# Kernel optimization log

Measured on AMD Instinct MI355X. Metric: run time of the kernel, lower is better.

## Reference

```python
import jax, jax.numpy as jnp
import numpy as np

# Module hyper-params (match init_kwargs)
IN_C, OUT_C = 64, 64
KH, KW = 3, 3            # kernel_size_2d
UNIT = 16                # unit_size (width of virtual 2D feature map)
K = KH * KW              # equivalent 1D kernel size = 9
PAD = (K - 1) // 2       # = 4


def _tap_positions(T):
    # Fixed integer deform-conv offsets: tap j in group g = j // KW gets
    # x-offset (UNIT - KW) * (g - center_group).
    center = (KH - 1) // 2
    off = np.array([(UNIT - KW) * (j // KW - center) for j in range(K)], dtype=np.int32)
    # deform-conv sample position for output t, tap j (stride=1, dilation=1):
    #   pos = t - PAD + j + off[j]
    pos = np.arange(T, dtype=np.int32)[None, :] - PAD + np.arange(K, dtype=np.int32)[:, None] + off[:, None]  # [K, T]
    valid = (pos >= 0) & (pos < T)
    return np.clip(pos, 0, T - 1), valid


def setup_inputs() -> dict:
    key = jax.random.key(0)
    k1, k2, k3 = jax.random.split(key, 3)
    B, T = 8, 65536
    x = jax.random.normal(k1, (B, IN_C, T), dtype=jnp.float32)
    # weight init: uniform(-stdv, stdv), stdv = 1/sqrt(in_c * 1 * K)
    stdv = 1.0 / float(np.sqrt(IN_C * K))
    weight = jax.random.uniform(k2, (OUT_C, IN_C, K), jnp.float32, -stdv, stdv)
    # bias init: uniform(-bound, bound), bound = 1/sqrt(fan_in) = stdv
    bias = jax.random.uniform(k3, (OUT_C,), jnp.float32, -stdv, stdv)
    return {"x": x, "weight": weight, "bias": bias}


def reference(x, weight, bias):
    B, C, T = x.shape
    pos, valid = _tap_positions(T)
    pos = jnp.asarray(pos)
    valid = jnp.asarray(valid)
    # integer gather (offsets are integer so bilinear sampling is exact), zero outside
    xg = jnp.where(valid[None, None], x[:, :, pos], 0.0)  # [B, C, K, T]
    out = jnp.einsum('ock,bckt->bot', weight, xg)          # [B, OUT_C, T]
    return out + bias[None, :, None]
```

## Files before the change

### kernel.cpp

```cpp
#include <hip/hip_runtime.h>


typedef short bf16x8 __attribute__((ext_vector_type(8)));
typedef short bf16x4 __attribute__((ext_vector_type(4)));
typedef float f32x4  __attribute__((ext_vector_type(4)));

#define T_LEN   65536
#define NT      128
#define ROWS    168
#define PITCH   68
#define LOFF    20
#define NCHUNK  18
#define OPITCH  132
#define XS_BYTES (ROWS * PITCH * 2)
#define OS_BYTES (32 * OPITCH * 4)
#define SMEM_BYTES XS_BYTES

__device__ __forceinline__ short f2bf(float f) {
    union { float f; unsigned u; } v; v.f = f;
    unsigned u = v.u;
    u += 0x7fffu + ((u >> 16) & 1u);
    return (short)(u >> 16);
}

__global__ void prep_w_kernel(const float* __restrict__ w, short* __restrict__ W2) {
    int idx = blockIdx.x * 256 + threadIdx.x;
    if (idx >= 4 * NCHUNK * 64) return;
    int lane = idx & 63;
    int g    = idx >> 6;
    int ch   = g >> 2;
    int mt   = g & 3;
    int o    = mt * 16 + (lane & 15);
    bf16x8 v;
#pragma unroll
    for (int i = 0; i < 8; ++i) {
        int kk = ch * 32 + (lane >> 4) * 8 + i;
        int j = kk >> 6, c = kk & 63;
        v[i] = f2bf(w[o * 576 + c * 9 + j]);
    }
    *(bf16x8*)(W2 + (size_t)idx * 8) = v;
}

__global__ __launch_bounds__(256, 4)
void ta_main_kernel(const float* __restrict__ x, const short* __restrict__ W2,
                    const float* __restrict__ bias, float* __restrict__ out) {
    __shared__ __align__(16) char smem[SMEM_BYTES];
    short* xs = (short*)smem;
    float* os = (float*)smem;

    const int tid  = threadIdx.x;
    const int wv   = tid >> 6;
    const int lane = tid & 63;
    const int l15  = lane & 15;
    const int quad = lane >> 4;
    const int b    = blockIdx.y;
    const int bxd  = blockIdx.x;
    const int bx   = (bxd & 7) * 64 + (bxd >> 3);
    const int t0   = bx * NT;

    const int c = tid >> 2;
    const int q = tid & 3;
    const float* xrow = x + (((size_t)(b * 64 + c)) << 16);
    const int tbase = t0 - LOFF;
    const bool interior = (t0 >= LOFF) && (t0 + (ROWS - LOFF) <= T_LEN);

    if (interior) {
        f32x4 v[11];
#pragma unroll
        for (int i = 0; i < 11; ++i) {
            const int f = q + 4 * i;
            if (f < 42) v[i] = *(const f32x4*)(xrow + tbase + 4 * f);
        }
#pragma unroll
        for (int i = 0; i < 11; ++i) {
            const int f = q + 4 * i;
            if (f < 42) {
                const int tt = 4 * f;
                xs[(tt + 0) * PITCH + c] = f2bf(v[i][0]);
                xs[(tt + 1) * PITCH + c] = f2bf(v[i][1]);
                xs[(tt + 2) * PITCH + c] = f2bf(v[i][2]);
                xs[(tt + 3) * PITCH + c] = f2bf(v[i][3]);
            }
        }
    } else {
#pragma unroll
        for (int i = 0; i < 11; ++i) {
            const int f = q + 4 * i;
            if (f < 42) {
                const int tt = 4 * f;
                const int tg = tbase + tt;
                f32x4 v;
                v[0] = ((unsigned)(tg + 0) < (unsigned)T_LEN) ? xrow[tg + 0] : 0.f;
                v[1] = ((unsigned)(tg + 1) < (unsigned)T_LEN) ? xrow[tg + 1] : 0.f;
                v[2] = ((unsigned)(tg + 2) < (unsigned)T_LEN) ? xrow[tg + 2] : 0.f;
                v[3] = ((unsigned)(tg + 3) < (unsigned)T_LEN) ? xrow[tg + 3] : 0.f;
                xs[(tt + 0) * PITCH + c] = f2bf(v[0]);
                xs[(tt + 1) * PITCH + c] = f2bf(v[1]);
                xs[(tt + 2) * PITCH + c] = f2bf(v[2]);
                xs[(tt + 3) * PITCH + c] = f2bf(v[3]);
            }
        }
    }
    __syncthreads();

    int bbase[2];
#pragma unroll
    for (int nt = 0; nt < 2; ++nt) {
        const int tl = wv * 32 + nt * 16 + l15;
        bbase[nt] = (tl + 3) * PITCH + quad * 8;
    }
    const short* w2p = W2 + (size_t)lane * 8;

    f32x4 acc[4][2] = {};

    const int dtab[9] = {-17, -16, -15, -1, 0, 1, 15, 16, 17};

    bf16x8 a_cur[4], b_cur[2], a_nxt[4], b_nxt[2];

    {
        const int roff0 = (dtab[0] + 17) * PITCH + 0;
#pragma unroll
        for (int mt = 0; mt < 4; ++mt)
            a_cur[mt] = *(const bf16x8*)(w2p + (size_t)(0 * 4 + mt) * 512);
#pragma unroll
        for (int nt = 0; nt < 2; ++nt) {
            union { bf16x8 v8; bf16x4 v4[2]; } u;
            u.v4[0] = *(const bf16x4*)(xs + bbase[nt] + roff0);
            u.v4[1] = *(const bf16x4*)(xs + bbase[nt] + roff0 + 4);
            b_cur[nt] = u.v8;
        }
    }

#pragma unroll
    for (int ch = 0; ch < NCHUNK; ++ch) {
        if (ch < NCHUNK - 1) {
            const int chn = ch + 1;
            const int jn = chn >> 1, hn = chn & 1;
            const int roffn = (dtab[jn] + 17) * PITCH + hn * 32;
#pragma unroll
            for (int mt = 0; mt < 4; ++mt)
                a_nxt[mt] = *(const bf16x8*)(w2p + (size_t)(chn * 4 + mt) * 512);
#pragma unroll
            for (int nt = 0; nt < 2; ++nt) {
                union { bf16x8 v8; bf16x4 v4[2]; } u;
                u.v4[0] = *(const bf16x4*)(xs + bbase[nt] + roffn);
                u.v4[1] = *(const bf16x4*)(xs + bbase[nt] + roffn + 4);
                b_nxt[nt] = u.v8;
            }
        }
#pragma unroll
        for (int mt = 0; mt < 4; ++mt)
#pragma unroll
            for (int nt = 0; nt < 2; ++nt)
                acc[mt][nt] = __builtin_amdgcn_mfma_f32_16x16x32_bf16(a_cur[mt], b_cur[nt], acc[mt][nt], 0, 0, 0);
        if (ch < NCHUNK - 1) {
#pragma unroll
            for (int mt = 0; mt < 4; ++mt) a_cur[mt] = a_nxt[mt];
#pragma unroll
            for (int nt = 0; nt < 2; ++nt) b_cur[nt] = b_nxt[nt];
        }
    }

    const size_t outb = ((size_t)(b * 64)) << 16;
#pragma unroll
    for (int p = 0; p < 2; ++p) {
        __syncthreads();
#pragma unroll
        for (int mtl = 0; mtl < 2; ++mtl) {
            const int mt = 2 * p + mtl;
#pragma unroll
            for (int r = 0; r < 4; ++r) {
                const int ol = mtl * 16 + quad * 4 + r;
                const float bv = bias[mt * 16 + quad * 4 + r];
#pragma unroll
                for (int nt = 0; nt < 2; ++nt) {
                    const int t = wv * 32 + nt * 16 + l15;
                    os[ol * OPITCH + t] = acc[mt][nt][r] + bv;
                }
            }
        }
        __syncthreads();
#pragma unroll
        for (int i = 0; i < 4; ++i) {
            const int item = tid + 256 * i;
            const int ol = item >> 5;
            const int f4 = item & 31;
            const f32x4 v = *(const f32x4*)(os + ol * OPITCH + 4 * f4);
            const int o = p * 32 + ol;
            *(f32x4*)(out + outb + (((size_t)o) << 16) + t0 + 4 * f4) = v;
        }
    }
}

extern "C" void kernel_launch(void* const* d_in, const int* in_sizes, int n_in,
                              void* d_out, int out_size, void* d_ws, size_t ws_size,
                              hipStream_t stream) {
    const float* x    = (const float*)d_in[0];
    const float* w    = (const float*)d_in[1];
    const float* bias = (const float*)d_in[2];
    float* out = (float*)d_out;
    short* W2  = (short*)d_ws;

    hipLaunchKernelGGL(prep_w_kernel, dim3(18), dim3(256), 0, stream, w, W2);
    hipLaunchKernelGGL(ta_main_kernel, dim3(T_LEN / NT, 8), dim3(256), 0, stream,
                       x, W2, bias, out);
}
```

Before: 263.7 us.

## Process four time tiles per block with double-buffered LDS prefetch of next tile

Each block now handles four consecutive 128-sample tiles. It issues the global loads for the next tile into registers before running the MFMA loop on the current one, then commits them to a second LDS buffer, so memory latency overlaps compute. The output staging through LDS is removed in favour of direct strided scalar stores of accumulators, and launch bounds drop to 3 blocks per SM to make room for the larger register and LDS footprint. The direct stores are only 16 lanes contiguous per row, which may coalesce worse than the previous float4 writes, and the grid shrinks to 1024 blocks.

```diff
diff --git a/kernel.cpp b/kernel.cpp
--- a/kernel.cpp
+++ b/kernel.cpp
@@ -7,14 +7,13 @@
 
 #define T_LEN   65536
 #define NT      128
+#define NTILE   4
+#define SPAN    (NT * NTILE)
 #define ROWS    168
 #define PITCH   68
 #define LOFF    20
 #define NCHUNK  18
-#define OPITCH  132
-#define XS_BYTES (ROWS * PITCH * 2)
-#define OS_BYTES (32 * OPITCH * 4)
-#define SMEM_BYTES XS_BYTES
+#define XS_SHORTS (ROWS * PITCH)
 
 __device__ __forceinline__ short f2bf(float f) {
     union { float f; unsigned u; } v; v.f = f;
@@ -41,12 +40,10 @@
     *(bf16x8*)(W2 + (size_t)idx * 8) = v;
 }
 
-__global__ __launch_bounds__(256, 4)
+__global__ __launch_bounds__(256, 3)
 void ta_main_kernel(const float* __restrict__ x, const short* __restrict__ W2,
                     const float* __restrict__ bias, float* __restrict__ out) {
-    __shared__ __align__(16) char smem[SMEM_BYTES];
-    short* xs = (short*)smem;
-    float* os = (float*)smem;
+    __shared__ __align__(16) short xsbuf[2][XS_SHORTS];
 
     const int tid  = threadIdx.x;
     const int wv   = tid >> 6;
@@ -55,52 +52,55 @@
     const int quad = lane >> 4;
     const int b    = blockIdx.y;
     const int bxd  = blockIdx.x;
-    const int bx   = (bxd & 7) * 64 + (bxd >> 3);
-    const int t0   = bx * NT;
+    const int bx   = (bxd & 7) * 16 + (bxd >> 3);
+    const int tg0  = bx * SPAN;
 
     const int c = tid >> 2;
     const int q = tid & 3;
     const float* xrow = x + (((size_t)(b * 64 + c)) << 16);
-    const int tbase = t0 - LOFF;
-    const bool interior = (t0 >= LOFF) && (t0 + (ROWS - LOFF) <= T_LEN);
-
-    if (interior) {
-        f32x4 v[11];
-#pragma unroll
-        for (int i = 0; i < 11; ++i) {
-            const int f = q + 4 * i;
-            if (f < 42) v[i] = *(const f32x4*)(xrow + tbase + 4 * f);
-        }
+
+    f32x4 v[11];
+
+    auto issue = [&](const int t0) {
+        const int tbase = t0 - LOFF;
+        if ((t0 >= LOFF) && (t0 + (ROWS - LOFF) <= T_LEN)) {
+#pragma unroll
+            for (int i = 0; i < 11; ++i) {
+                const int f = q + 4 * i;
+                if (f < 42) v[i] = *(const f32x4*)(xrow + tbase + 4 * f);
+            }
+        } else {
+#pragma unroll
+            for (int i = 0; i < 11; ++i) {
+                const int f = q + 4 * i;
+                if (f < 42) {
+                    const int tg = tbase + 4 * f;
+                    f32x4 t;
+                    t[0] = ((unsigned)(tg + 0) < (unsigned)T_LEN) ? xrow[tg + 0] : 0.f;
+                    t[1] = ((unsigned)(tg + 1) < (unsigned)T_LEN) ? xrow[tg + 1] : 0.f;
+                    t[2] = ((unsigned)(tg + 2) < (unsigned)T_LEN) ? xrow[tg + 2] : 0.f;
+                    t[3] = ((unsigned)(tg + 3) < (unsigned)T_LEN) ? xrow[tg + 3] : 0.f;
+                    v[i] = t;
+                }
+            }
+        }
+    };
+    auto commit = [&](short* dst) {
 #pragma unroll
         for (int i = 0; i < 11; ++i) {
             const int f = q + 4 * i;
             if (f < 42) {
                 const int tt = 4 * f;
-                xs[(tt + 0) * PITCH + c] = f2bf(v[i][0]);
-                xs[(tt + 1) * PITCH + c] = f2bf(v[i][1]);
-                xs[(tt + 2) * PITCH + c] = f2bf(v[i][2]);
-                xs[(tt + 3) * PITCH + c] = f2bf(v[i][3]);
-            }
-        }
-    } else {
-#pragma unroll
-        for (int i = 0; i < 11; ++i) {
-            const int f = q + 4 * i;
-            if (f < 42) {
-                const int tt = 4 * f;
-                const int tg = tbase + tt;
-                f32x4 v;
-                v[0] = ((unsigned)(tg + 0) < (unsigned)T_LEN) ? xrow[tg + 0] : 0.f;
-                v[1] = ((unsigned)(tg + 1) < (unsigned)T_LEN) ? xrow[tg + 1] : 0.f;
-                v[2] = ((unsigned)(tg + 2) < (unsigned)T_LEN) ? xrow[tg + 2] : 0.f;
-                v[3] = ((unsigned)(tg + 3) < (unsigned)T_LEN) ? xrow[tg + 3] : 0.f;
-                xs[(tt + 0) * PITCH + c] = f2bf(v[0]);
-                xs[(tt + 1) * PITCH + c] = f2bf(v[1]);
-                xs[(tt + 2) * PITCH + c] = f2bf(v[2]);
-                xs[(tt + 3) * PITCH + c] = f2bf(v[3]);
-            }
-        }
-    }
+                dst[(tt + 0) * PITCH + c] = f2bf(v[i][0]);
+                dst[(tt + 1) * PITCH + c] = f2bf(v[i][1]);
+                dst[(tt + 2) * PITCH + c] = f2bf(v[i][2]);
+                dst[(tt + 3) * PITCH + c] = f2bf(v[i][3]);
+            }
+        }
+    };
+
+    issue(tg0);
+    commit(xsbuf[0]);
     __syncthreads();
 
     int bbase[2];
@@ -110,85 +110,86 @@
         bbase[nt] = (tl + 3) * PITCH + quad * 8;
     }
     const short* w2p = W2 + (size_t)lane * 8;
-
-    f32x4 acc[4][2] = {};
-
+    const size_t outb = ((size_t)(b * 64)) << 16;
     const int dtab[9] = {-17, -16, -15, -1, 0, 1, 15, 16, 17};
 
-    bf16x8 a_cur[4], b_cur[2], a_nxt[4], b_nxt[2];
-
-    {
-        const int roff0 = (dtab[0] + 17) * PITCH + 0;
-#pragma unroll
-        for (int mt = 0; mt < 4; ++mt)
-            a_cur[mt] = *(const bf16x8*)(w2p + (size_t)(0 * 4 + mt) * 512);
-#pragma unroll
-        for (int nt = 0; nt < 2; ++nt) {
-            union { bf16x8 v8; bf16x4 v4[2]; } u;
-            u.v4[0] = *(const bf16x4*)(xs + bbase[nt] + roff0);
-            u.v4[1] = *(const bf16x4*)(xs + bbase[nt] + roff0 + 4);
-            b_cur[nt] = u.v8;
-        }
-    }
-
-#pragma unroll
-    for (int ch = 0; ch < NCHUNK; ++ch) {
-        if (ch < NCHUNK - 1) {
-            const int chn = ch + 1;
-            const int jn = chn >> 1, hn = chn & 1;
-            const int roffn = (dtab[jn] + 17) * PITCH + hn * 32;
-#pragma unroll
-            for (int mt = 0; mt < 4; ++mt)
-                a_nxt[mt] = *(const bf16x8*)(w2p + (size_t)(chn * 4 + mt) * 512);
+    short* cur = xsbuf[0];
+    short* nxt = xsbuf[1];
+
+#pragma unroll
+    for (int it = 0; it < NTILE; ++it) {
+        const int t0 = tg0 + it * NT;
+        const bool more = (it + 1 < NTILE);
+
+        if (more) issue(t0 + NT);
+        __builtin_amdgcn_sched_barrier(0);
+
+        f32x4 acc[4][2] = {};
+        bf16x8 a_cur[4], b_cur[2], a_nxt[4], b_nxt[2];
+        {
+            const int roff0 = (dtab[0] + 17) * PITCH + 0;
+#pragma unroll
+            for (int mt = 0; mt < 4; ++mt)
+                a_cur[mt] = *(const bf16x8*)(w2p + (size_t)(0 * 4 + mt) * 512);
 #pragma unroll
             for (int nt = 0; nt < 2; ++nt) {
                 union { bf16x8 v8; bf16x4 v4[2]; } u;
-                u.v4[0] = *(const bf16x4*)(xs + bbase[nt] + roffn);
-                u.v4[1] = *(const bf16x4*)(xs + bbase[nt] + roffn + 4);
-                b_nxt[nt] = u.v8;
-            }
-        }
-#pragma unroll
-        for (int mt = 0; mt < 4; ++mt)
-#pragma unroll
-            for (int nt = 0; nt < 2; ++nt)
-                acc[mt][nt] = __builtin_amdgcn_mfma_f32_16x16x32_bf16(a_cur[mt], b_cur[nt], acc[mt][nt], 0, 0, 0);
-        if (ch < NCHUNK - 1) {
-#pragma unroll
-            for (int mt = 0; mt < 4; ++mt) a_cur[mt] = a_nxt[mt];
-#pragma unroll
-            for (int nt = 0; nt < 2; ++nt) b_cur[nt] = b_nxt[nt];
-        }
-    }
-
-    const size_t outb = ((size_t)(b * 64)) << 16;
-#pragma unroll
-    for (int p = 0; p < 2; ++p) {
+                u.v4[0] = *(const bf16x4*)(cur + bbase[nt] + roff0);
+                u.v4[1] = *(const bf16x4*)(cur + bbase[nt] + roff0 + 4);
+                b_cur[nt] = u.v8;
+            }
+        }
+#pragma unroll
+        for (int ch = 0; ch < NCHUNK; ++ch) {
+            if (ch < NCHUNK - 1) {
+                const int chn = ch + 1;
+                const int jn = chn >> 1, hn = chn & 1;
+                const int roffn = (dtab[jn] + 17) * PITCH + hn * 32;
+#pragma unroll
+                for (int mt = 0; mt < 4; ++mt)
+                    a_nxt[mt] = *(const bf16x8*)(w2p + (size_t)(chn * 4 + mt) * 512);
+#pragma unroll
+                for (int nt = 0; nt < 2; ++nt) {
+                    union { bf16x8 v8; bf16x4 v4[2]; } u;
+                    u.v4[0] = *(const bf16x4*)(cur + bbase[nt] + roffn);
+                    u.v4[1] = *(const bf16x4*)(cur + bbase[nt] + roffn + 4);
+                    b_nxt[nt] = u.v8;
+                }
+            }
+#pragma unroll
+            for (int mt = 0; mt < 4; ++mt)
+#pragma unroll
+                for (int nt = 0; nt < 2; ++nt)
+                    acc[mt][nt] = __builtin_amdgcn_mfma_f32_16x16x32_bf16(a_cur[mt], b_cur[nt], acc[mt][nt], 0, 0, 0);
+            if (ch < NCHUNK - 1) {
+#pragma unroll
+                for (int mt = 0; mt < 4; ++mt) a_cur[mt] = a_nxt[mt];
+#pragma unroll
+                for (int nt = 0; nt < 2; ++nt) b_cur[nt] = b_nxt[nt];
+            }
+        }
+
+        if (more) commit(nxt);
+
+        {
+            f32x4 bv[4];
+#pragma unroll
+            for (int mt = 0; mt < 4; ++mt)
+                bv[mt] = *(const f32x4*)(bias + mt * 16 + quad * 4);
+            float* obase = out + outb + t0 + wv * 32 + l15;
+#pragma unroll
+            for (int mt = 0; mt < 4; ++mt)
+#pragma unroll
+                for (int r = 0; r < 4; ++r) {
+                    const int orow = (mt * 16 + quad * 4 + r) << 16;
+#pragma unroll
+                    for (int nt = 0; nt < 2; ++nt)
+                        obase[orow + nt * 16] = acc[mt][nt][r] + bv[mt][r];
+                }
+        }
+
         __syncthreads();
-#pragma unroll
-        for (int mtl = 0; mtl < 2; ++mtl) {
-            const int mt = 2 * p + mtl;
-#pragma unroll
-            for (int r = 0; r < 4; ++r) {
-                const int ol = mtl * 16 + quad * 4 + r;
-                const float bv = bias[mt * 16 + quad * 4 + r];
-#pragma unroll
-                for (int nt = 0; nt < 2; ++nt) {
-                    const int t = wv * 32 + nt * 16 + l15;
-                    os[ol * OPITCH + t] = acc[mt][nt][r] + bv;
-                }
-            }
-        }
-        __syncthreads();
-#pragma unroll
-        for (int i = 0; i < 4; ++i) {
-            const int item = tid + 256 * i;
-            const int ol = item >> 5;
-            const int f4 = item & 31;
-            const f32x4 v = *(const f32x4*)(os + ol * OPITCH + 4 * f4);
-            const int o = p * 32 + ol;
-            *(f32x4*)(out + outb + (((size_t)o) << 16) + t0 + 4 * f4) = v;
-        }
+        short* tmp = cur; cur = nxt; nxt = tmp;
     }
 }
 
@@ -202,6 +203,6 @@
     short* W2  = (short*)d_ws;
 
     hipLaunchKernelGGL(prep_w_kernel, dim3(18), dim3(256), 0, stream, w, W2);
-    hipLaunchKernelGGL(ta_main_kernel, dim3(T_LEN / NT, 8), dim3(256), 0, stream,
+    hipLaunchKernelGGL(ta_main_kernel, dim3(T_LEN / SPAN, 8), dim3(256), 0, stream,
                        x, W2, bias, out);
 }
```

Result: slower. 449.6 us (+70.5%).
